# Performance work log

Measured on AMD Instinct MI355X. Metric: run time of the kernel, lower is better.

## Reference

```python
import jax, jax.numpy as jnp
import numpy as np

NEG = jnp.float32(-1e30)  # log-space 'zero' (safer than -inf under jit/grad)
ALPHA = 0.5
GAMMA = 2.0
BLANK = 0


def _ctc_loss_mean(log_probs, targets, input_lengths, target_lengths):
    # log_probs: [T, N, C] (already log-softmaxed), targets: [N, S] (labels >= 1)
    T, N, C = log_probs.shape
    S = targets.shape[1]
    L = 2 * S + 1  # extended target: blank-interleaved

    # extended targets: even positions = blank, odd = labels
    ext = jnp.zeros((N, L), dtype=jnp.int32).at[:, 1::2].set(targets.astype(jnp.int32))
    l_idx = jnp.arange(L)
    valid = l_idx[None, :] < (2 * target_lengths + 1)[:, None]  # [N, L]
    ext_m2 = jnp.pad(ext, ((0, 0), (2, 0)))[:, :L]
    can_skip = (l_idx[None, :] >= 2) & (ext != BLANK) & (ext != ext_m2)  # [N, L]

    # gather per-frame log-probs of extended labels: [T, N, L] (small lattice)
    lp_ext = jnp.take_along_axis(log_probs, jnp.broadcast_to(ext[None], (T, N, L)), axis=2)

    # alpha at t=0
    alpha0 = jnp.full((N, L), NEG)
    alpha0 = alpha0.at[:, 0].set(lp_ext[0, :, 0]).at[:, 1].set(lp_ext[0, :, 1])
    alpha0 = jnp.where(valid, alpha0, NEG)

    def step(alpha, x):
        lp_t, t = x
        a1 = alpha
        a2 = jnp.pad(alpha, ((0, 0), (1, 0)), constant_values=NEG)[:, :L]
        a3 = jnp.where(can_skip, jnp.pad(alpha, ((0, 0), (2, 0)), constant_values=NEG)[:, :L], NEG)
        m = jnp.maximum(jnp.maximum(a1, a2), a3)
        new = m + jnp.log(jnp.exp(a1 - m) + jnp.exp(a2 - m) + jnp.exp(a3 - m)) + lp_t
        new = jnp.where(valid, new, NEG)
        # freeze alpha once past this sample's input length
        alpha = jnp.where((t < input_lengths)[:, None], new, alpha)
        return alpha, None

    alphaT, _ = jax.lax.scan(step, alpha0, (lp_ext[1:], jnp.arange(1, T)))

    i1 = (2 * target_lengths)[:, None]
    i2 = (2 * target_lengths - 1)[:, None]
    a1 = jnp.take_along_axis(alphaT, i1, axis=1)[:, 0]
    a2 = jnp.take_along_axis(alphaT, i2, axis=1)[:, 0]
    loss = -jnp.logaddexp(a1, a2)  # [N]
    # zero_infinity=True: infeasible alignments -> 0
    loss = jnp.where(loss > 1e29, 0.0, loss)
    # reduction='mean': divide by target lengths, then mean over batch
    return jnp.mean(loss / target_lengths.astype(loss.dtype))


def setup_inputs() -> dict:
    key = jax.random.key(0)
    k1, k2, k3 = jax.random.split(key, 3)
    T, N, C, S = 160, 128, 6625, 32
    log_probs = jax.nn.log_softmax(jax.random.normal(k1, (T, N, C), dtype=jnp.float32), axis=-1)
    targets = jax.random.randint(k2, (N, S), 1, C).astype(jnp.int32)  # labels exclude blank=0
    input_lengths = jnp.full((N,), T, dtype=jnp.int32)
    target_lengths = jax.random.randint(k3, (N,), 16, S + 1).astype(jnp.int32)
    return {"log_probs": log_probs, "targets": targets,
            "input_lengths": input_lengths, "target_lengths": target_lengths}


def reference(log_probs, targets, input_lengths, target_lengths):
    loss_ctc = _ctc_loss_mean(log_probs, targets, input_lengths, target_lengths)
    p = jnp.exp(-loss_ctc)
    return ALPHA * (1.0 - p) ** GAMMA * loss_ctc
```

## Files before the change

kernel.cpp:

```cpp
#include <hip/hip_runtime.h>
#include <math.h>


#define TT 160
#define NN 128
#define CC 6625
#define SS 32
#define JJ 33
#define NTJ (TT * JJ)
#define CHT 32
#define CHE (CHT * JJ)
#define NCH 5
#define NEGV  (-1e30f)
#define LOG2E 1.4426950408889634f
#define LN2   0.6931471805599453f

__device__ __forceinline__ float dpp_up1(float x, bool row0lane) {
    int xi = __float_as_int(x);
    int shr = __builtin_amdgcn_update_dpp(xi, xi, 0x111, 0xf, 0xf, false);
    int bc  = __builtin_amdgcn_update_dpp(xi, xi, 0x142, 0xf, 0xf, false);
    return __int_as_float(row0lane ? bc : shr);
}

__global__ __launch_bounds__(1024) void ctc_fused_kernel(
    const float* __restrict__ log_probs,
    const int*   __restrict__ targets,
    const int*   __restrict__ input_lengths,
    const int*   __restrict__ target_lengths,
    float*       __restrict__ per_sample)
{
    const int n   = blockIdx.x;
    const int tid = threadIdx.x;

    __shared__ float lp[NTJ];
    __shared__ int   lab[JJ];

    if (tid < JJ) lab[tid] = (tid == 0) ? 0 : targets[n * SS + tid - 1];
    __syncthreads();

    const size_t rowbase = (size_t)n * CC;

#pragma unroll
    for (int k = 0; k < 2; ++k) {
        const int i = tid + k * 1024;
        if (i < CHE) {
            const int t = i / JJ;
            const int j = i - t * JJ;
            lp[i] = log_probs[(size_t)t * (NN * CC) + rowbase + lab[j]] * LOG2E;
        }
    }
    __syncthreads();

    const int lane = tid;
    const int tl = target_lengths[n];
    const int Lv = 2 * tl + 1;
    const int slot = (lane & 1) ? (1 + (lane >> 1)) : 0;
    const bool skip = (lane & 1) && (lane >= 3) &&
                      (lab[(lane >> 1) < SS ? 1 + (lane >> 1) : 1] !=
                       lab[(lane >> 1) < 1 ? 0 : (lane >> 1)]);
    const bool validl   = lane < Lv;
    const bool valid64  = 64 < Lv;
    const bool row0lane = (lane & 15) == 0;

    float v = NEGV;
    if (lane == 0) v = lp[0];
    if (lane == 1) v = lp[1];
    float e = NEGV;

    const int ilen = input_lengths[n];
    const int Tlim = (ilen < TT) ? ilen : TT;

    for (int c = 0; c < NCH; ++c) {
        if (tid >= 64 && c + 1 < NCH) {
            const int base = (c + 1) * CHE;
#pragma unroll
            for (int k = 0; k < 2; ++k) {
                const int r = (tid - 64) + k * 960;
                if (r < CHE) {
                    const int i = base + r;
                    const int t = i / JJ;
                    const int j = i - t * JJ;
                    lp[i] = log_probs[(size_t)t * (NN * CC) + rowbase + lab[j]] * LOG2E;
                }
            }
        }
        if (tid < 64) {
            const int t_lo = (c == 0) ? 1 : c * CHT;
            int t_hi = (c + 1) * CHT;
            if (t_hi > Tlim) t_hi = Tlim;
            for (int t = t_lo; t < t_hi; ++t) {
                const float u1 = dpp_up1(v, row0lane);
                const float u2 = dpp_up1(u1, row0lane);
                const float a2 = (lane == 0) ? NEGV : u1;
                const float a3 = skip ? u2 : NEGV;

                const float lpt64 = lp[t * JJ];
                const float me = fmaxf(e, v);
                const float ne = me + log2f(exp2f(e - me) + exp2f(v - me)) + lpt64;

                const float m  = fmaxf(v, fmaxf(a2, a3));
                const float nv = m + log2f(exp2f(v - m) + exp2f(a2 - m) + exp2f(a3 - m))
                                   + lp[t * JJ + slot];

                v = validl  ? nv : NEGV;
                e = valid64 ? ne : NEGV;
            }
        }
        __syncthreads();
    }

    if (tid >= 64) return;

    const int i1 = 2 * tl;
    const int i2 = 2 * tl - 1;
    const float A1 = (i1 == 64) ? __shfl(e, 63) : __shfl(v, i1);
    const float A2 = __shfl(v, i2);
    if (lane == 0) {
        const float m = fmaxf(A1, A2);
        float loss = -LN2 * (m + log2f(exp2f(A1 - m) + exp2f(A2 - m)));
        if (loss > 1e29f) loss = 0.0f;
        per_sample[n] = loss / (float)tl;
    }
}

__global__ __launch_bounds__(128) void focal_reduce_kernel(
    const float* __restrict__ per_sample, float* __restrict__ out)
{
    __shared__ float s[NN];
    int tid = threadIdx.x;
    s[tid] = per_sample[tid];
    __syncthreads();
    for (int off = NN / 2; off > 0; off >>= 1) {
        if (tid < off) s[tid] += s[tid + off];
        __syncthreads();
    }
    if (tid == 0) {
        float mean = s[0] / (float)NN;
        float pp = expf(-mean);
        float om = 1.0f - pp;
        out[0] = 0.5f * om * om * mean;
    }
}

extern "C" void kernel_launch(void* const* d_in, const int* in_sizes, int n_in,
                              void* d_out, int out_size, void* d_ws, size_t ws_size,
                              hipStream_t stream) {
    const float* log_probs      = (const float*)d_in[0];
    const int*   targets        = (const int*)d_in[1];
    const int*   input_lengths  = (const int*)d_in[2];
    const int*   target_lengths = (const int*)d_in[3];
    float* out        = (float*)d_out;
    float* per_sample = (float*)d_ws;

    ctc_fused_kernel<<<NN, 1024, 0, stream>>>(log_probs, targets, input_lengths,
                                              target_lengths, per_sample);
    focal_reduce_kernel<<<1, NN, 0, stream>>>(per_sample, out);
}
```

Measured before the change: 39.66 us.

## Split scattered log-prob gather into separate kernel, stream contiguous workspace into scan

Moves the random-access gather of extended-label log-probs out of the scan kernel into a separate fully parallel kernel that writes a contiguous per-sample workspace. The scan kernel then copies chunks with float4 loads, overlapping later chunks with the recurrence as before. The goal is to spread the latency-bound scattered gather across many more threads and blocks than the 128 scan blocks provide. In exchange it adds a kernel launch and a round trip through global memory. The skip-mask indexing is also rewritten in a form that is equivalent for the 64 active lanes.

```diff
diff --git a/kernel.cpp b/kernel.cpp
--- a/kernel.cpp
+++ b/kernel.cpp
@@ -10,6 +10,7 @@
 #define NTJ (TT * JJ)
 #define CHT 32
 #define CHE (CHT * JJ)
+#define CH4 (CHE / 4)
 #define NCH 5
 #define NEGV  (-1e30f)
 #define LOG2E 1.4426950408889634f
@@ -22,8 +23,22 @@
     return __int_as_float(row0lane ? bc : shr);
 }
 
-__global__ __launch_bounds__(1024) void ctc_fused_kernel(
+__global__ __launch_bounds__(256) void gather_ws_kernel(
     const float* __restrict__ log_probs,
+    const int*   __restrict__ targets,
+    float*       __restrict__ lp_ws)
+{
+    const int g = blockIdx.x * 256 + threadIdx.x;
+    const int n = g / NTJ;
+    const int r = g - n * NTJ;
+    const int t = r / JJ;
+    const int j = r - t * JJ;
+    const int label = j ? targets[n * SS + j - 1] : 0;
+    lp_ws[g] = log_probs[(size_t)t * (NN * CC) + (size_t)n * CC + label] * LOG2E;
+}
+
+__global__ __launch_bounds__(1024) void scan_kernel(
+    const float* __restrict__ lp_ws,
     const int*   __restrict__ targets,
     const int*   __restrict__ input_lengths,
     const int*   __restrict__ target_lengths,
@@ -36,19 +51,10 @@
     __shared__ int   lab[JJ];
 
     if (tid < JJ) lab[tid] = (tid == 0) ? 0 : targets[n * SS + tid - 1];
-    __syncthreads();
 
-    const size_t rowbase = (size_t)n * CC;
-
-#pragma unroll
-    for (int k = 0; k < 2; ++k) {
-        const int i = tid + k * 1024;
-        if (i < CHE) {
-            const int t = i / JJ;
-            const int j = i - t * JJ;
-            lp[i] = log_probs[(size_t)t * (NN * CC) + rowbase + lab[j]] * LOG2E;
-        }
-    }
+    const float4* s4 = (const float4*)(lp_ws + (size_t)n * NTJ);
+    float4* d4 = (float4*)lp;
+    if (tid < CH4) d4[tid] = s4[tid];
     __syncthreads();
 
     const int lane = tid;
@@ -56,8 +62,7 @@
     const int Lv = 2 * tl + 1;
     const int slot = (lane & 1) ? (1 + (lane >> 1)) : 0;
     const bool skip = (lane & 1) && (lane >= 3) &&
-                      (lab[(lane >> 1) < SS ? 1 + (lane >> 1) : 1] !=
-                       lab[(lane >> 1) < 1 ? 0 : (lane >> 1)]);
+                      (lab[(lane & 63) >> 1 ? 1 + (lane >> 1) : 1] != lab[(lane >> 1) ? (lane >> 1) : 1]);
     const bool validl   = lane < Lv;
     const bool valid64  = 64 < Lv;
     const bool row0lane = (lane & 15) == 0;
@@ -71,17 +76,11 @@
     const int Tlim = (ilen < TT) ? ilen : TT;
 
     for (int c = 0; c < NCH; ++c) {
-        if (tid >= 64 && c + 1 < NCH) {
-            const int base = (c + 1) * CHE;
-#pragma unroll
-            for (int k = 0; k < 2; ++k) {
-                const int r = (tid - 64) + k * 960;
-                if (r < CHE) {
-                    const int i = base + r;
-                    const int t = i / JJ;
-                    const int j = i - t * JJ;
-                    lp[i] = log_probs[(size_t)t * (NN * CC) + rowbase + lab[j]] * LOG2E;
-                }
+        if (c + 1 < NCH) {
+            const int r = tid - 64;
+            if (r >= 0 && r < CH4) {
+                const int i = (c + 1) * CH4 + r;
+                d4[i] = s4[i];
             }
         }
         if (tid < 64) {
@@ -149,10 +148,13 @@
     const int*   targets        = (const int*)d_in[1];
     const int*   input_lengths  = (const int*)d_in[2];
     const int*   target_lengths = (const int*)d_in[3];
-    float* out        = (float*)d_out;
+    float* out = (float*)d_out;
+
     float* per_sample = (float*)d_ws;
+    float* lp_ws      = (float*)((char*)d_ws + 1024);
 
-    ctc_fused_kernel<<<NN, 1024, 0, stream>>>(log_probs, targets, input_lengths,
-                                              target_lengths, per_sample);
+    gather_ws_kernel<<<(NN * NTJ) / 256, 256, 0, stream>>>(log_probs, targets, lp_ws);
+    scan_kernel<<<NN, 1024, 0, stream>>>(lp_ws, targets, input_lengths,
+                                         target_lengths, per_sample);
     focal_reduce_kernel<<<1, NN, 0, stream>>>(per_sample, out);
 }
```

Result: slower. 50.72 us (+27.9%).
